# Optimization experiments

Hardware: AMD Instinct MI355X
Metric: run time of the kernel (lower is better)

The kernel has to match this reference:

```python
import jax, jax.numpy as jnp
import numpy as np

D1, K, B, C, T = 270, 32, 128, 273, 1024
KAIMING_BOUND = 1.0 / 32.0  # sqrt(6/((1+5)*K*K)) for a=sqrt(5), fan_in=K*K=1024


def setup_inputs() -> dict:
    key = jax.random.key(0)
    k1, k2, k3, k4 = jax.random.split(key, 4)
    X = jax.random.normal(k1, (B, C, T), dtype=jnp.float32)
    loc = jax.random.uniform(k2, (C, 2), dtype=jnp.float32)  # normalized 2D sensor coords
    z_re = jax.random.uniform(k3, (D1, K, K), minval=-KAIMING_BOUND, maxval=KAIMING_BOUND, dtype=jnp.float32)
    z_im = jax.random.uniform(k4, (D1, K, K), minval=-KAIMING_BOUND, maxval=KAIMING_BOUND, dtype=jnp.float32)
    return {"X": X, "loc": loc, "z_re": z_re, "z_im": z_im}


def reference(X, loc, z_re, z_im):
    # Algebraic rewrite of the D1*K*K python loop:
    # a[j,c] = sum_{k,l} z_re[j,k,l]*cos(2pi(k*x_c + l*y_c)) + z_im[j,k,l]*sin(...)
    x, y = loc[:, 0], loc[:, 1]                    # [C]
    k = jnp.arange(K, dtype=loc.dtype)
    phase = 2.0 * jnp.pi * (k[:, None, None] * x[None, None, :]
                            + k[None, :, None] * y[None, None, :])  # [K, K, C]
    a = (jnp.einsum('jkl,klc->jc', z_re, jnp.cos(phase))
         + jnp.einsum('jkl,klc->jc', z_im, jnp.sin(phase)))          # [D1, C]
    e = jnp.exp(a)
    w = e / jnp.sum(e, axis=1, keepdims=True)      # exp-normalized channel weights
    # out[b,j,t] = sum_c w[j,c] * X[b,c,t]  (stack over j + permute(1,0,2) in original)
    return jnp.einsum('jc,bct->bjt', w, X)
```

## Files before the change

### kernel.cpp

```cpp
#include <hip/hip_runtime.h>
#include <hip/hip_bf16.h>

#define NUM_D1 270
#define NUM_B  128
#define NUM_C  273
#define NUM_T  1024
#define KL     1024
#define TW     320
#define CP     288
#define CW     296
#define ROWB   (CW * 2)

#define WT_BYTES (144 * ROWB)
#define XB_BYTES (64 * ROWB)
#define LDS5_TOTAL (WT_BYTES + 2 * XB_BYTES)

typedef float f32x4 __attribute__((ext_vector_type(4)));
typedef __bf16 bf16x8 __attribute__((ext_vector_type(8)));

static __device__ __forceinline__ unsigned short f2bf(float f) {
  unsigned u = __float_as_uint(f);
  unsigned r = (u + 0x7fffu + ((u >> 16) & 1u)) >> 16;
  return (unsigned short)r;
}

__global__ __launch_bounds__(256) void k_trig(const float* __restrict__ loc,
                                              float* __restrict__ cosT,
                                              float* __restrict__ sinT) {
  int idx = blockIdx.x * 256 + threadIdx.x;
  int kl = idx / TW;
  int c  = idx - kl * TW;
  float cv = 0.f, sv = 0.f;
  if (c < NUM_C) {
    float x = loc[2 * c], y = loc[2 * c + 1];
    float kf = (float)(kl >> 5), lf = (float)(kl & 31);
    float ph = 6.283185307179586f * (kf * x + lf * y);
    sincosf(ph, &sv, &cv);
  }
  cosT[idx] = cv;
  sinT[idx] = sv;
}

__global__ __launch_bounds__(1024) void k_agemm(const float* __restrict__ z_re,
                                                const float* __restrict__ z_im,
                                                const float* __restrict__ cosT,
                                                const float* __restrict__ sinT,
                                                float* __restrict__ a) {
  __shared__ float sm[4][8][64];
  int tid = threadIdx.x;
  int lane = tid & 63;
  int g = tid >> 6;
  int p = g >> 3;
  int q = g & 7;
  int jb = blockIdx.x;
  int cb = blockIdx.y;
  int c = cb * 64 + lane;
  int j_a = jb * 4 + p;
  int j_b = j_a + 2;
  int jeb = (j_b < NUM_D1) ? j_b : 0;
  const float* zr0 = z_re + (size_t)j_a * KL;
  const float* zi0 = z_im + (size_t)j_a * KL;
  const float* zr1 = z_re + (size_t)jeb * KL;
  const float* zi1 = z_im + (size_t)jeb * KL;
  float a0 = 0.f, a1 = 0.f;
  int k0 = q * 128;
  #pragma unroll 4
  for (int kk = k0; kk < k0 + 128; ++kk) {
    float cv = cosT[kk * TW + c];
    float sv = sinT[kk * TW + c];
    a0 = fmaf(zr0[kk], cv, a0);
    a0 = fmaf(zi0[kk], sv, a0);
    a1 = fmaf(zr1[kk], cv, a1);
    a1 = fmaf(zi1[kk], sv, a1);
  }
  sm[p][q][lane] = a0;
  sm[p + 2][q][lane] = a1;
  __syncthreads();
  if (tid < 256) {
    int jl = tid >> 6;
    int l2 = tid & 63;
    int j = jb * 4 + jl;
    int c2 = cb * 64 + l2;
    float s = 0.f;
    #pragma unroll
    for (int qq = 0; qq < 8; ++qq) s += sm[jl][qq][l2];
    if (j < NUM_D1 && c2 < NUM_C) a[j * CP + c2] = s;
  }
}

__global__ __launch_bounds__(256) void k_softmax(const float* __restrict__ a,
                                                 unsigned short* __restrict__ wg) {
  int wv = threadIdx.x >> 6;
  int lane = threadIdx.x & 63;
  int j = blockIdx.x * 4 + wv;
  if (j >= NUM_D1) {
    for (int c = lane; c < CW; c += 64) wg[j * CW + c] = 0;
    return;
  }
  float e[5];
  float s = 0.f;
  #pragma unroll
  for (int qq = 0; qq < 5; ++qq) {
    int c = qq * 64 + lane;
    float v = 0.f;
    if (c < NUM_C) v = expf(a[j * CP + c]);
    e[qq] = v;
    s += v;
  }
  #pragma unroll
  for (int o = 32; o > 0; o >>= 1) s += __shfl_xor(s, o, 64);
  float inv = 1.0f / s;
  #pragma unroll
  for (int qq = 0; qq < 5; ++qq) {
    int c = qq * 64 + lane;
    if (c < CW) wg[j * CW + c] = (c < NUM_C) ? f2bf(e[qq] * inv) : (unsigned short)0;
  }
}

__global__ __launch_bounds__(768, 3) void k_out5(const float* __restrict__ X,
                                                 const unsigned short* __restrict__ wg,
                                                 float* __restrict__ out) {
  extern __shared__ char lds[];
  char* WTb = lds;
  char* XA  = lds + WT_BYTES;
  char* XBf = lds + WT_BYTES + XB_BYTES;

  const int tid = threadIdx.x;
  const int wv = tid >> 6, lane = tid & 63;
  const int rlo = lane & 15, kg = lane >> 4;

  const int lin = blockIdx.x;
  const int xcd = lin & 7, slot = lin >> 3;
  const int jh = slot & 1;
  const int b  = xcd * 16 + (slot >> 1);

  const float* Xb = X + (size_t)b * (NUM_C * NUM_T);

  const int co = tid >> 4;
  const int t4 = tid & 15;
  const bool stg = (co < 36);
  const int swz = (t4 & 3) << 4;

  const int tt = wv & 3, jq = wv >> 2;
  const int t = tt * 16 + rlo;
  const int sw = ((t >> 2) & 3) << 4;

  f32x4 va[8];
  if (stg) {
    #pragma unroll
    for (int e = 0; e < 8; ++e) {
      int c = co * 8 + e;
      if (c < NUM_C) va[e] = *(const f32x4*)(Xb + (size_t)c * NUM_T + t4 * 4);
      else { va[e][0] = va[e][1] = va[e][2] = va[e][3] = 0.f; }
    }
  }
  {
    const char* wsrc = (const char*)wg + (size_t)jh * WT_BYTES;
    #pragma unroll
    for (int i = 0; i < 7; ++i) {
      int off = (tid + i * 768) * 16;
      if (off < WT_BYTES) *(uint4*)(WTb + off) = *(const uint4*)(wsrc + off);
    }
  }
  if (stg) {
    #pragma unroll
    for (int f = 0; f < 4; ++f) {
      int tw = t4 * 4 + f;
      ushort4 p0, p1;
      p0.x = f2bf(va[0][f]); p0.y = f2bf(va[1][f]);
      p0.z = f2bf(va[2][f]); p0.w = f2bf(va[3][f]);
      p1.x = f2bf(va[4][f]); p1.y = f2bf(va[5][f]);
      p1.z = f2bf(va[6][f]); p1.w = f2bf(va[7][f]);
      *(ushort4*)(XA + tw * ROWB + ((co * 16) ^ swz)) = p0;
      *(ushort4*)(XA + tw * ROWB + ((co * 16 + 8) ^ swz)) = p1;
    }
  }
  __syncthreads();

  for (int it = 0; it < 16; ++it) {
    const int t0 = it * 64;
    char* xcur = (it & 1) ? XBf : XA;
    char* xnxt = (it & 1) ? XA : XBf;
    const bool pf = stg && (it < 15);

    if (pf) {
      #pragma unroll
      for (int e = 0; e < 8; ++e) {
        int c = co * 8 + e;
        if (c < NUM_C) va[e] = *(const f32x4*)(Xb + (size_t)c * NUM_T + t0 + 64 + t4 * 4);
        else { va[e][0] = va[e][1] = va[e][2] = va[e][3] = 0.f; }
      }
    }
    __builtin_amdgcn_sched_barrier(0);

    f32x4 acc[3];
    #pragma unroll
    for (int jt = 0; jt < 3; ++jt)
      acc[jt][0] = acc[jt][1] = acc[jt][2] = acc[jt][3] = 0.f;

    #pragma unroll
    for (int ks = 0; ks < 9; ++ks) {
      bf16x8 bfr = *(const bf16x8*)(xcur + t * ROWB + ((ks * 64 + kg * 16) ^ sw));
      #pragma unroll
      for (int jt = 0; jt < 3; ++jt) {
        bf16x8 afr = *(const bf16x8*)(WTb +
            (size_t)((jq * 3 + jt) * 16 + rlo) * ROWB + kg * 16 + ks * 64);
        acc[jt] = __builtin_amdgcn_mfma_f32_16x16x32_bf16(afr, bfr, acc[jt], 0, 0, 0);
      }
    }

    #pragma unroll
    for (int jt = 0; jt < 3; ++jt) {
      #pragma unroll
      for (int r = 0; r < 4; ++r) {
        int j = jh * 144 + (jq * 3 + jt) * 16 + kg * 4 + r;
        if (j < NUM_D1)
          out[((size_t)b * NUM_D1 + j) * NUM_T + t0 + t] = acc[jt][r];
      }
    }

    if (it < 15) {
      asm volatile("s_waitcnt vmcnt(12)" ::: "memory");
      __builtin_amdgcn_sched_barrier(0);
      if (pf) {
        #pragma unroll
        for (int f = 0; f < 4; ++f) {
          int tw = t4 * 4 + f;
          ushort4 p0, p1;
          p0.x = f2bf(va[0][f]); p0.y = f2bf(va[1][f]);
          p0.z = f2bf(va[2][f]); p0.w = f2bf(va[3][f]);
          p1.x = f2bf(va[4][f]); p1.y = f2bf(va[5][f]);
          p1.z = f2bf(va[6][f]); p1.w = f2bf(va[7][f]);
          *(ushort4*)(xnxt + tw * ROWB + ((co * 16) ^ swz)) = p0;
          *(ushort4*)(xnxt + tw * ROWB + ((co * 16 + 8) ^ swz)) = p1;
        }
      }
      asm volatile("s_waitcnt lgkmcnt(0)" ::: "memory");
      __builtin_amdgcn_sched_barrier(0);
      __builtin_amdgcn_s_barrier();
      __builtin_amdgcn_sched_barrier(0);
    }
  }
}

extern "C" void kernel_launch(void* const* d_in, const int* in_sizes, int n_in,
                              void* d_out, int out_size, void* d_ws, size_t ws_size,
                              hipStream_t stream) {
  const float* X   = (const float*)d_in[0];
  const float* loc = (const float*)d_in[1];
  const float* zre = (const float*)d_in[2];
  const float* zim = (const float*)d_in[3];
  float* out = (float*)d_out;
  char* ws = (char*)d_ws;
  float* cosT = (float*)(ws);
  float* sinT = (float*)(ws + 1310720);
  float* a    = (float*)(ws + 2621440);
  unsigned short* wgp = (unsigned short*)(ws + 2934784);

  (void)hipFuncSetAttribute((const void*)k_out5,
                            hipFuncAttributeMaxDynamicSharedMemorySize, LDS5_TOTAL);

  hipLaunchKernelGGL(k_trig,    dim3(1280),   dim3(256),  0, stream, loc, cosT, sinT);
  hipLaunchKernelGGL(k_agemm,   dim3(68, 5),  dim3(1024), 0, stream, zre, zim, cosT, sinT, a);
  hipLaunchKernelGGL(k_softmax, dim3(72),     dim3(256),  0, stream, a, wgp);
  hipLaunchKernelGGL(k_out5,    dim3(256),    dim3(768),  LDS5_TOTAL, stream, X, wgp, out);
}
```

Before: 133.3 us.

## Warp-specialize output GEMM into producer and MFMA waves; interleave trig table

The output kernel is split by wave role. Three waves run the MFMAs, each covering 48 rows by 64 time steps with register-blocked A/B fragment reuse. The other nine waves act as producers that load X, convert it with the packed v_cvt_pk_bf16 instruction, and stage it into double-buffered LDS two iterations ahead. The LDS XOR swizzle is removed. The cos/sin tables are interleaved into one float2 array so the coefficient GEMM issues one load per step. This risks leaving only three waves for matrix work and may add LDS bank conflicts now that the swizzle is gone.

```diff
diff --git a/kernel.cpp b/kernel.cpp
--- a/kernel.cpp
+++ b/kernel.cpp
@@ -13,10 +13,18 @@
 
 #define WT_BYTES (144 * ROWB)
 #define XB_BYTES (64 * ROWB)
-#define LDS5_TOTAL (WT_BYTES + 2 * XB_BYTES)
+#define LDS6_TOTAL (WT_BYTES + 2 * XB_BYTES)
 
 typedef float f32x4 __attribute__((ext_vector_type(4)));
 typedef __bf16 bf16x8 __attribute__((ext_vector_type(8)));
+
+#define FENCED_BARRIER()                                     \
+  do {                                                       \
+    asm volatile("s_waitcnt lgkmcnt(0)" ::: "memory");       \
+    __builtin_amdgcn_s_barrier();                            \
+    asm volatile("" ::: "memory");                           \
+    __builtin_amdgcn_sched_barrier(0);                       \
+  } while (0)
 
 static __device__ __forceinline__ unsigned short f2bf(float f) {
   unsigned u = __float_as_uint(f);
@@ -24,9 +32,14 @@
   return (unsigned short)r;
 }
 
+static __device__ __forceinline__ unsigned cvt_pk_bf16(float lo, float hi) {
+  unsigned r;
+  asm("v_cvt_pk_bf16_f32 %0, %1, %2" : "=v"(r) : "v"(lo), "v"(hi));
+  return r;
+}
+
 __global__ __launch_bounds__(256) void k_trig(const float* __restrict__ loc,
-                                              float* __restrict__ cosT,
-                                              float* __restrict__ sinT) {
+                                              float2* __restrict__ tab) {
   int idx = blockIdx.x * 256 + threadIdx.x;
   int kl = idx / TW;
   int c  = idx - kl * TW;
@@ -37,14 +50,12 @@
     float ph = 6.283185307179586f * (kf * x + lf * y);
     sincosf(ph, &sv, &cv);
   }
-  cosT[idx] = cv;
-  sinT[idx] = sv;
+  tab[idx] = make_float2(cv, sv);
 }
 
 __global__ __launch_bounds__(1024) void k_agemm(const float* __restrict__ z_re,
                                                 const float* __restrict__ z_im,
-                                                const float* __restrict__ cosT,
-                                                const float* __restrict__ sinT,
+                                                const float2* __restrict__ tab,
                                                 float* __restrict__ a) {
   __shared__ float sm[4][8][64];
   int tid = threadIdx.x;
@@ -66,12 +77,11 @@
   int k0 = q * 128;
   #pragma unroll 4
   for (int kk = k0; kk < k0 + 128; ++kk) {
-    float cv = cosT[kk * TW + c];
-    float sv = sinT[kk * TW + c];
-    a0 = fmaf(zr0[kk], cv, a0);
-    a0 = fmaf(zi0[kk], sv, a0);
-    a1 = fmaf(zr1[kk], cv, a1);
-    a1 = fmaf(zi1[kk], sv, a1);
+    float2 cs = tab[kk * TW + c];
+    a0 = fmaf(zr0[kk], cs.x, a0);
+    a0 = fmaf(zi0[kk], cs.y, a0);
+    a1 = fmaf(zr1[kk], cs.x, a1);
+    a1 = fmaf(zi1[kk], cs.y, a1);
   }
   sm[p][q][lane] = a0;
   sm[p + 2][q][lane] = a1;
@@ -117,7 +127,7 @@
   }
 }
 
-__global__ __launch_bounds__(768, 3) void k_out5(const float* __restrict__ X,
+__global__ __launch_bounds__(768, 3) void k_out6(const float* __restrict__ X,
                                                  const unsigned short* __restrict__ wg,
                                                  float* __restrict__ out) {
   extern __shared__ char lds[];
@@ -128,25 +138,21 @@
   const int tid = threadIdx.x;
   const int wv = tid >> 6, lane = tid & 63;
   const int rlo = lane & 15, kg = lane >> 4;
+  const bool isProd = (wv >= 3);
 
   const int lin = blockIdx.x;
   const int xcd = lin & 7, slot = lin >> 3;
   const int jh = slot & 1;
   const int b  = xcd * 16 + (slot >> 1);
-
   const float* Xb = X + (size_t)b * (NUM_C * NUM_T);
 
-  const int co = tid >> 4;
-  const int t4 = tid & 15;
-  const bool stg = (co < 36);
-  const int swz = (t4 & 3) << 4;
-
-  const int tt = wv & 3, jq = wv >> 2;
-  const int t = tt * 16 + rlo;
-  const int sw = ((t >> 2) & 3) << 4;
+  const int s  = isProd ? (tid - 192) : 0;
+  const int t4 = s / 36;
+  const int co = s - t4 * 36;
 
   f32x4 va[8];
-  if (stg) {
+
+  if (isProd) {
     #pragma unroll
     for (int e = 0; e < 8; ++e) {
       int c = co * 8 + e;
@@ -162,84 +168,93 @@
       if (off < WT_BYTES) *(uint4*)(WTb + off) = *(const uint4*)(wsrc + off);
     }
   }
-  if (stg) {
+  if (isProd) {
     #pragma unroll
     for (int f = 0; f < 4; ++f) {
-      int tw = t4 * 4 + f;
-      ushort4 p0, p1;
-      p0.x = f2bf(va[0][f]); p0.y = f2bf(va[1][f]);
-      p0.z = f2bf(va[2][f]); p0.w = f2bf(va[3][f]);
-      p1.x = f2bf(va[4][f]); p1.y = f2bf(va[5][f]);
-      p1.z = f2bf(va[6][f]); p1.w = f2bf(va[7][f]);
-      *(ushort4*)(XA + tw * ROWB + ((co * 16) ^ swz)) = p0;
-      *(ushort4*)(XA + tw * ROWB + ((co * 16 + 8) ^ swz)) = p1;
-    }
-  }
-  __syncthreads();
+      uint4 w;
+      w.x = cvt_pk_bf16(va[0][f], va[1][f]);
+      w.y = cvt_pk_bf16(va[2][f], va[3][f]);
+      w.z = cvt_pk_bf16(va[4][f], va[5][f]);
+      w.w = cvt_pk_bf16(va[6][f], va[7][f]);
+      *(uint4*)(XA + (t4 * 4 + f) * ROWB + co * 16) = w;
+    }
+    #pragma unroll
+    for (int e = 0; e < 8; ++e) {
+      int c = co * 8 + e;
+      if (c < NUM_C) va[e] = *(const f32x4*)(Xb + (size_t)c * NUM_T + 64 + t4 * 4);
+      else { va[e][0] = va[e][1] = va[e][2] = va[e][3] = 0.f; }
+    }
+  }
+  FENCED_BARRIER();
+
+  const int jq = wv;
 
   for (int it = 0; it < 16; ++it) {
     const int t0 = it * 64;
     char* xcur = (it & 1) ? XBf : XA;
     char* xnxt = (it & 1) ? XA : XBf;
-    const bool pf = stg && (it < 15);
-
-    if (pf) {
+
+    if (!isProd) {
+      f32x4 acc[3][4];
       #pragma unroll
-      for (int e = 0; e < 8; ++e) {
-        int c = co * 8 + e;
-        if (c < NUM_C) va[e] = *(const f32x4*)(Xb + (size_t)c * NUM_T + t0 + 64 + t4 * 4);
-        else { va[e][0] = va[e][1] = va[e][2] = va[e][3] = 0.f; }
+      for (int jt = 0; jt < 3; ++jt)
+        #pragma unroll
+        for (int tt = 0; tt < 4; ++tt)
+          acc[jt][tt][0] = acc[jt][tt][1] = acc[jt][tt][2] = acc[jt][tt][3] = 0.f;
+
+      const char* wbase = WTb + (size_t)(jq * 48 + rlo) * ROWB + kg * 16;
+      const char* xbase = xcur + (size_t)rlo * ROWB + kg * 16;
+
+      #pragma unroll
+      for (int ks = 0; ks < 9; ++ks) {
+        bf16x8 a0 = *(const bf16x8*)(wbase + 0 * 16 * ROWB + ks * 64);
+        bf16x8 a1 = *(const bf16x8*)(wbase + 1 * 16 * ROWB + ks * 64);
+        bf16x8 a2 = *(const bf16x8*)(wbase + 2 * 16 * ROWB + ks * 64);
+        #pragma unroll
+        for (int tt = 0; tt < 4; ++tt) {
+          bf16x8 bq = *(const bf16x8*)(xbase + tt * 16 * ROWB + ks * 64);
+          acc[0][tt] = __builtin_amdgcn_mfma_f32_16x16x32_bf16(a0, bq, acc[0][tt], 0, 0, 0);
+          acc[1][tt] = __builtin_amdgcn_mfma_f32_16x16x32_bf16(a1, bq, acc[1][tt], 0, 0, 0);
+          acc[2][tt] = __builtin_amdgcn_mfma_f32_16x16x32_bf16(a2, bq, acc[2][tt], 0, 0, 0);
+        }
       }
-    }
-    __builtin_amdgcn_sched_barrier(0);
-
-    f32x4 acc[3];
-    #pragma unroll
-    for (int jt = 0; jt < 3; ++jt)
-      acc[jt][0] = acc[jt][1] = acc[jt][2] = acc[jt][3] = 0.f;
-
-    #pragma unroll
-    for (int ks = 0; ks < 9; ++ks) {
-      bf16x8 bfr = *(const bf16x8*)(xcur + t * ROWB + ((ks * 64 + kg * 16) ^ sw));
+
       #pragma unroll
       for (int jt = 0; jt < 3; ++jt) {
-        bf16x8 afr = *(const bf16x8*)(WTb +
-            (size_t)((jq * 3 + jt) * 16 + rlo) * ROWB + kg * 16 + ks * 64);
-        acc[jt] = __builtin_amdgcn_mfma_f32_16x16x32_bf16(afr, bfr, acc[jt], 0, 0, 0);
+        int jb2 = jh * 144 + (jq * 3 + jt) * 16 + kg * 4;
+        #pragma unroll
+        for (int tt = 0; tt < 4; ++tt) {
+          #pragma unroll
+          for (int r = 0; r < 4; ++r) {
+            int j = jb2 + r;
+            if (j < NUM_D1)
+              out[((size_t)b * NUM_D1 + j) * NUM_T + t0 + tt * 16 + rlo] = acc[jt][tt][r];
+          }
+        }
       }
-    }
-
-    #pragma unroll
-    for (int jt = 0; jt < 3; ++jt) {
-      #pragma unroll
-      for (int r = 0; r < 4; ++r) {
-        int j = jh * 144 + (jq * 3 + jt) * 16 + kg * 4 + r;
-        if (j < NUM_D1)
-          out[((size_t)b * NUM_D1 + j) * NUM_T + t0 + t] = acc[jt][r];
+    } else {
+      if (it < 15) {
+        #pragma unroll
+        for (int f = 0; f < 4; ++f) {
+          uint4 w;
+          w.x = cvt_pk_bf16(va[0][f], va[1][f]);
+          w.y = cvt_pk_bf16(va[2][f], va[3][f]);
+          w.z = cvt_pk_bf16(va[4][f], va[5][f]);
+          w.w = cvt_pk_bf16(va[6][f], va[7][f]);
+          *(uint4*)(xnxt + (t4 * 4 + f) * ROWB + co * 16) = w;
+        }
+        if (it < 14) {
+          #pragma unroll
+          for (int e = 0; e < 8; ++e) {
+            int c = co * 8 + e;
+            if (c < NUM_C) va[e] = *(const f32x4*)(Xb + (size_t)c * NUM_T + t0 + 128 + t4 * 4);
+            else { va[e][0] = va[e][1] = va[e][2] = va[e][3] = 0.f; }
+          }
+        }
       }
     }
 
-    if (it < 15) {
-      asm volatile("s_waitcnt vmcnt(12)" ::: "memory");
-      __builtin_amdgcn_sched_barrier(0);
-      if (pf) {
-        #pragma unroll
-        for (int f = 0; f < 4; ++f) {
-          int tw = t4 * 4 + f;
-          ushort4 p0, p1;
-          p0.x = f2bf(va[0][f]); p0.y = f2bf(va[1][f]);
-          p0.z = f2bf(va[2][f]); p0.w = f2bf(va[3][f]);
-          p1.x = f2bf(va[4][f]); p1.y = f2bf(va[5][f]);
-          p1.z = f2bf(va[6][f]); p1.w = f2bf(va[7][f]);
-          *(ushort4*)(xnxt + tw * ROWB + ((co * 16) ^ swz)) = p0;
-          *(ushort4*)(xnxt + tw * ROWB + ((co * 16 + 8) ^ swz)) = p1;
-        }
-      }
-      asm volatile("s_waitcnt lgkmcnt(0)" ::: "memory");
-      __builtin_amdgcn_sched_barrier(0);
-      __builtin_amdgcn_s_barrier();
-      __builtin_amdgcn_sched_barrier(0);
-    }
+    FENCED_BARRIER();
   }
 }
 
@@ -252,16 +267,15 @@
   const float* zim = (const float*)d_in[3];
   float* out = (float*)d_out;
   char* ws = (char*)d_ws;
-  float* cosT = (float*)(ws);
-  float* sinT = (float*)(ws + 1310720);
+  float2* tab = (float2*)(ws);
   float* a    = (float*)(ws + 2621440);
   unsigned short* wgp = (unsigned short*)(ws + 2934784);
 
-  (void)hipFuncSetAttribute((const void*)k_out5,
-                            hipFuncAttributeMaxDynamicSharedMemorySize, LDS5_TOTAL);
-
-  hipLaunchKernelGGL(k_trig,    dim3(1280),   dim3(256),  0, stream, loc, cosT, sinT);
-  hipLaunchKernelGGL(k_agemm,   dim3(68, 5),  dim3(1024), 0, stream, zre, zim, cosT, sinT, a);
+  (void)hipFuncSetAttribute((const void*)k_out6,
+                            hipFuncAttributeMaxDynamicSharedMemorySize, LDS6_TOTAL);
+
+  hipLaunchKernelGGL(k_trig,    dim3(1280),   dim3(256),  0, stream, loc, tab);
+  hipLaunchKernelGGL(k_agemm,   dim3(68, 5),  dim3(1024), 0, stream, zre, zim, tab, a);
   hipLaunchKernelGGL(k_softmax, dim3(72),     dim3(256),  0, stream, a, wgp);
-  hipLaunchKernelGGL(k_out5,    dim3(256),    dim3(768),  LDS5_TOTAL, stream, X, wgp, out);
-}
+  hipLaunchKernelGGL(k_out6,    dim3(256),    dim3(768),  LDS6_TOTAL, stream, X, wgp, out);
+}
```

Measured after the change: 204.8 us. +53.7%, slower.
